# Optimization experiments

Hardware: AMD Instinct MI355X
Metric: run time of the kernel (lower is better)

## Reference

```python
import jax, jax.numpy as jnp
import numpy as np

N, D_IN, D_BLOCK, D_OUT, E, K = 65536, 128, 256, 128, 8, 2


def setup_inputs() -> dict:
    key = jax.random.key(0)
    ks = jax.random.split(key, 8)
    s_in = 1.0 / np.sqrt(D_IN)
    s_h = 1.0 / np.sqrt(D_BLOCK)
    return {
        "x": jax.random.normal(ks[0], (N, D_IN), jnp.float32),
        "Wg": jax.random.normal(ks[1], (D_IN, E), jnp.float32) * s_in,
        "W1": jax.random.normal(ks[2], (E, D_IN, D_BLOCK), jnp.float32) * s_in,
        "b1": jax.random.normal(ks[3], (E, D_BLOCK), jnp.float32) * 0.01,
        "W2": jax.random.normal(ks[4], (E, D_BLOCK, D_BLOCK), jnp.float32) * s_h,
        "b2": jax.random.normal(ks[5], (E, D_BLOCK), jnp.float32) * 0.01,
        "Wo": jax.random.normal(ks[6], (D_BLOCK, D_OUT), jnp.float32) * s_h,
        "bo": jax.random.normal(ks[7], (D_OUT,), jnp.float32) * 0.01,
    }


def reference(x, Wg, W1, b1, W2, b2, Wo, bo):
    # Router: linear gate -> top-k -> softmax over the k selected logits,
    # scattered back to a dense [N, E] combine-weight matrix (zeros elsewhere).
    logits = x @ Wg                                   # [N, E]
    topv, topi = jax.lax.top_k(logits, K)             # [N, K]
    w_topk = jax.nn.softmax(topv, axis=-1)            # [N, K]
    onehot = jax.nn.one_hot(topi, E, dtype=x.dtype)   # [N, K, E]
    weights = jnp.einsum("nk,nke->ne", w_topk, onehot)  # [N, E]

    # Expert MLPs (n_blocks=2, ReLU, dropout=0 at eval), computed for all
    # experts over all tokens; unselected experts have weight 0, so the
    # weighted combine reproduces the original masked gather/scatter math.
    h = jax.nn.relu(jnp.einsum("nd,edh->enh", x, W1) + b1[:, None, :])   # [E,N,H]
    h = jax.nn.relu(jnp.einsum("enh,ehg->eng", h, W2) + b2[:, None, :])  # [E,N,H]
    y = jnp.einsum("enh,ho->eno", h, Wo) + bo                             # [E,N,O]

    # Weighted scatter-add combine: outs[n] = sum_e weights[n,e] * y[e,n]
    return jnp.einsum("ne,eno->no", weights, y)
```

## Files before the change

### kernel.cpp

```cpp
#include <hip/hip_runtime.h>
#include <math.h>

typedef unsigned short ushort_t;
typedef __attribute__((ext_vector_type(8))) short bf16x8;
typedef __attribute__((ext_vector_type(4))) float f32x4;
typedef __attribute__((ext_vector_type(8))) unsigned short u16x8;

#define N_TOK 65536
#define DIN 128
#define HD 256
#define DOUT 128
#define NEXP 8
#define MT 64
#define NSEG 32
#define SEGCAP 2048
#define SEGTILES (SEGCAP / MT)

__device__ __forceinline__ unsigned short f2bf(float f) {
    union { float f; unsigned int i; } v; v.f = f;
    unsigned int i = v.i;
    return (unsigned short)((i + 0x7FFFu + ((i >> 16) & 1u)) >> 16);
}

__global__ void pack_weights(const float* __restrict__ W1,
                             const float* __restrict__ W2,
                             const float* __restrict__ Wo,
                             ushort_t* __restrict__ wt1f,
                             ushort_t* __restrict__ wt2f,
                             ushort_t* __restrict__ wotf,
                             int* __restrict__ segcnt) {
    if (blockIdx.x == 0) segcnt[threadIdx.x] = 0;
    int id = blockIdx.x * 256 + threadIdx.x;
    const float* src; ushort_t* dst; int Nn, ksteps, c;
    if (id < 32768) {
        int e = id >> 12; c = id & 4095;
        Nn = HD; ksteps = 4; src = W1 + (size_t)e * DIN * HD; dst = wt1f + (size_t)id * 8;
    } else if (id < 98304) {
        int t = id - 32768; int e = t >> 13; c = t & 8191;
        Nn = HD; ksteps = 8; src = W2 + (size_t)e * HD * HD; dst = wt2f + (size_t)t * 8;
    } else {
        int t = id - 98304; c = t;
        Nn = DOUT; ksteps = 8; src = Wo; dst = wotf + (size_t)t * 8;
    }
    int L = c & 63; int kc = c >> 6;
    int kstep = kc % ksteps; int ntile = kc / ksteps;
    int q = L >> 4, m = L & 15;
    int n = ntile * 16 + m; int k0 = kstep * 32 + q * 8;
    u16x8 v;
#pragma unroll
    for (int j = 0; j < 8; j++) v[j] = f2bf(src[(size_t)(k0 + j) * Nn + n]);
    *(u16x8*)dst = v;
}

#define RT_TPB 32
__global__ __launch_bounds__(256)
void router_kernel(const float* __restrict__ x,
                   const float* __restrict__ Wg,
                   int* __restrict__ segcnt,
                   int* __restrict__ list_tok,
                   float* __restrict__ list_w) {
    __shared__ float wgsT[NEXP * 132];
    __shared__ int lcnt[NEXP];
    __shared__ int lbase[NEXP];
    int tid = threadIdx.x;
    if (tid < NEXP) lcnt[tid] = 0;
    for (int i = tid; i < DIN * NEXP; i += 256) {
        int e = i & 7, k = i >> 3;
        wgsT[e * 132 + k] = Wg[i];
    }
    __syncthreads();

    int s = tid & 7;
    int tl = tid >> 3;
    int n = blockIdx.x * RT_TPB + tl;

    const float4* xr = (const float4*)(x + (size_t)n * DIN + s * 16);
    float4 xv[4];
#pragma unroll
    for (int j = 0; j < 4; j++) xv[j] = xr[j];

    float lg[NEXP];
#pragma unroll
    for (int e = 0; e < NEXP; e++) {
        const float4* wp = (const float4*)(wgsT + e * 132 + s * 16);
        float a = 0.f;
#pragma unroll
        for (int j = 0; j < 4; j++) {
            float4 wv = wp[j];
            a += xv[j].x * wv.x + xv[j].y * wv.y + xv[j].z * wv.z + xv[j].w * wv.w;
        }
        lg[e] = a;
    }
#pragma unroll
    for (int d = 1; d < 8; d <<= 1) {
#pragma unroll
        for (int e = 0; e < NEXP; e++) lg[e] += __shfl_xor(lg[e], d, 64);
    }
    int e0 = 0; float v0 = lg[0];
#pragma unroll
    for (int e = 1; e < NEXP; e++) if (lg[e] > v0) { v0 = lg[e]; e0 = e; }
    int e1 = -1; float v1 = -3.0e38f;
#pragma unroll
    for (int e = 0; e < NEXP; e++) if (e != e0 && lg[e] > v1) { v1 = lg[e]; e1 = e; }
    float t = expf(v1 - v0);
    float inv = 1.0f / (1.0f + t);
    float w0 = inv, w1 = t * inv;

    bool writer = (s == 0);
    int p0 = 0, p1 = 0;
    if (writer) {
        p0 = atomicAdd(&lcnt[e0], 1);
        p1 = atomicAdd(&lcnt[e1], 1);
    }
    __syncthreads();
    int c = blockIdx.x & (NSEG - 1);
    if (tid < NEXP) lbase[tid] = atomicAdd(&segcnt[tid * NSEG + c], lcnt[tid]);
    __syncthreads();
    if (writer) {
        int q0 = lbase[e0] + p0;
        int idx0 = (e0 * NSEG + c) * SEGCAP + q0;
        list_tok[idx0] = n;
        list_w[idx0] = w0;
        int q1 = lbase[e1] + p1;
        int idx1 = (e1 * NSEG + c) * SEGCAP + q1;
        list_tok[idx1] = n;
        list_w[idx1] = w1;
    }
}

__global__ void init_out(const float* __restrict__ bo, float* __restrict__ out) {
    int gid = blockIdx.x * 256 + threadIdx.x;
    float4 b = ((const float4*)bo)[gid & 31];
    ((float4*)out)[gid] = b;
}

__global__ __launch_bounds__(256, 3)
void expert_kernel(const float* __restrict__ x,
                   const int* __restrict__ segcnt,
                   const int* __restrict__ list_tok,
                   const float* __restrict__ list_w,
                   const ushort_t* __restrict__ wt1f,
                   const ushort_t* __restrict__ wt2f,
                   const ushort_t* __restrict__ wotf,
                   const float* __restrict__ b1,
                   const float* __restrict__ b2,
                   float* __restrict__ out) {
    int bid = blockIdx.x;
    int e = bid & 7;
    int c = (bid >> 3) & (NSEG - 1);
    int t = bid >> 8;
    int cnt = segcnt[e * NSEG + c];
    int base = t * MT;
    if (base >= cnt) return;
    int rows = cnt - base; if (rows > MT) rows = MT;
    int lidx = (e * NSEG + c) * SEGCAP + base;

    __shared__ __align__(16) ushort_t bufA[8192];
    __shared__ __align__(16) ushort_t bufH[16384];
    __shared__ int toks_s[MT];
    __shared__ float wts_s[MT];

    int tid = threadIdx.x;
    int lane = tid & 63;
    int w = tid >> 6;
    int q = lane >> 4;
    int mcol = lane & 15;

    if (tid < MT) {
        int rr = tid < rows ? tid : rows - 1;
        toks_s[tid] = list_tok[lidx + rr];
        wts_s[tid] = list_w[lidx + rr];
    }
    for (int cc = tid; cc < 1024; cc += 256) {
        int row = cc >> 4;
        int kchunk = cc & 15;
        int rr = row < rows ? row : rows - 1;
        int tok = list_tok[lidx + rr];
        const float4* src = (const float4*)(x + (size_t)tok * DIN + kchunk * 8);
        float4 lo = src[0], hi = src[1];
        u16x8 v;
        v[0] = f2bf(lo.x); v[1] = f2bf(lo.y); v[2] = f2bf(lo.z); v[3] = f2bf(lo.w);
        v[4] = f2bf(hi.x); v[5] = f2bf(hi.y); v[6] = f2bf(hi.z); v[7] = f2bf(hi.w);
        int kstep = kchunk >> 2, qq = kchunk & 3;
        int dchunk = (kstep * 4 + (row >> 4)) * 64 + qq * 16 + (row & 15);
        ((u16x8*)bufA)[dchunk] = v;
    }
    __syncthreads();

    const bf16x8* Albs = (const bf16x8*)bufA;
    const bf16x8* Hlbs = (const bf16x8*)bufH;

    f32x4 acc[4][4];
#pragma unroll
    for (int mt = 0; mt < 4; mt++)
#pragma unroll
        for (int nt = 0; nt < 4; nt++) acc[mt][nt] = (f32x4){0.f, 0.f, 0.f, 0.f};
    const bf16x8* B1 = (const bf16x8*)(wt1f + (size_t)e * 4096 * 8);
#pragma unroll
    for (int kstep = 0; kstep < 4; kstep++) {
        bf16x8 a[4];
#pragma unroll
        for (int mt = 0; mt < 4; mt++) a[mt] = Albs[(kstep * 4 + mt) * 64 + lane];
#pragma unroll
        for (int nt = 0; nt < 4; nt++) {
            bf16x8 b = B1[((w * 4 + nt) * 4 + kstep) * 64 + lane];
#pragma unroll
            for (int mt = 0; mt < 4; mt++)
                acc[mt][nt] = __builtin_amdgcn_mfma_f32_16x16x32_bf16(a[mt], b, acc[mt][nt], 0, 0, 0);
        }
    }
#pragma unroll
    for (int nt = 0; nt < 4; nt++) {
        int nn = (w * 4 + nt) * 16 + mcol;
        float bias = b1[e * HD + nn];
        int kstep = nn >> 5, qq = (nn >> 3) & 3, jj = nn & 7;
#pragma unroll
        for (int mt = 0; mt < 4; mt++) {
#pragma unroll
            for (int r = 0; r < 4; r++) {
                float v = acc[mt][nt][r] + bias;
                v = v > 0.f ? v : 0.f;
                int chunk = (kstep * 4 + mt) * 64 + qq * 16 + q * 4 + r;
                bufH[chunk * 8 + jj] = f2bf(v);
            }
        }
    }
    __syncthreads();

    f32x4 acc2[4][4];
#pragma unroll
    for (int mt = 0; mt < 4; mt++)
#pragma unroll
        for (int nt = 0; nt < 4; nt++) acc2[mt][nt] = (f32x4){0.f, 0.f, 0.f, 0.f};
    const bf16x8* B2 = (const bf16x8*)(wt2f + (size_t)e * 8192 * 8);
#pragma unroll
    for (int kstep = 0; kstep < 8; kstep++) {
        bf16x8 a[4];
#pragma unroll
        for (int mt = 0; mt < 4; mt++) a[mt] = Hlbs[(kstep * 4 + mt) * 64 + lane];
#pragma unroll
        for (int nt = 0; nt < 4; nt++) {
            bf16x8 b = B2[((w * 4 + nt) * 8 + kstep) * 64 + lane];
#pragma unroll
            for (int mt = 0; mt < 4; mt++)
                acc2[mt][nt] = __builtin_amdgcn_mfma_f32_16x16x32_bf16(a[mt], b, acc2[mt][nt], 0, 0, 0);
        }
    }
    __syncthreads();
#pragma unroll
    for (int nt = 0; nt < 4; nt++) {
        int nn = (w * 4 + nt) * 16 + mcol;
        float bias = b2[e * HD + nn];
        int kstep = nn >> 5, qq = (nn >> 3) & 3, jj = nn & 7;
#pragma unroll
        for (int mt = 0; mt < 4; mt++) {
#pragma unroll
            for (int r = 0; r < 4; r++) {
                float v = acc2[mt][nt][r] + bias;
                v = v > 0.f ? v : 0.f;
                int chunk = (kstep * 4 + mt) * 64 + qq * 16 + q * 4 + r;
                bufH[chunk * 8 + jj] = f2bf(v);
            }
        }
    }
    __syncthreads();

    f32x4 acc3[4][2];
#pragma unroll
    for (int mt = 0; mt < 4; mt++)
#pragma unroll
        for (int nt = 0; nt < 2; nt++) acc3[mt][nt] = (f32x4){0.f, 0.f, 0.f, 0.f};
    const bf16x8* B3 = (const bf16x8*)wotf;
#pragma unroll
    for (int kstep = 0; kstep < 8; kstep++) {
        bf16x8 a[4];
#pragma unroll
        for (int mt = 0; mt < 4; mt++) a[mt] = Hlbs[(kstep * 4 + mt) * 64 + lane];
#pragma unroll
        for (int nt = 0; nt < 2; nt++) {
            bf16x8 b = B3[((w * 2 + nt) * 8 + kstep) * 64 + lane];
#pragma unroll
            for (int mt = 0; mt < 4; mt++)
                acc3[mt][nt] = __builtin_amdgcn_mfma_f32_16x16x32_bf16(a[mt], b, acc3[mt][nt], 0, 0, 0);
        }
    }
#pragma unroll
    for (int mt = 0; mt < 4; mt++) {
#pragma unroll
        for (int r = 0; r < 4; r++) {
            int row = mt * 16 + q * 4 + r;
            if (row < rows) {
                int tok = toks_s[row];
                float wgt = wts_s[row];
                float* dst = out + (size_t)tok * DOUT;
#pragma unroll
                for (int nt = 0; nt < 2; nt++) {
                    int col = (w * 2 + nt) * 16 + mcol;
                    atomicAdd(&dst[col], wgt * acc3[mt][nt][r]);
                }
            }
        }
    }
}

extern "C" void kernel_launch(void* const* d_in, const int* in_sizes, int n_in,
                              void* d_out, int out_size, void* d_ws, size_t ws_size,
                              hipStream_t stream) {
    const float* x  = (const float*)d_in[0];
    const float* Wg = (const float*)d_in[1];
    const float* W1 = (const float*)d_in[2];
    const float* b1 = (const float*)d_in[3];
    const float* W2 = (const float*)d_in[4];
    const float* b2 = (const float*)d_in[5];
    const float* Wo = (const float*)d_in[6];
    const float* bo = (const float*)d_in[7];
    float* out = (float*)d_out;

    char* ws = (char*)d_ws;
    size_t off = 0;
    int* segcnt    = (int*)(ws + off);    off += 1024;
    int* list_tok  = (int*)(ws + off);    off += (size_t)NEXP * NSEG * SEGCAP * 4;
    float* list_w  = (float*)(ws + off);  off += (size_t)NEXP * NSEG * SEGCAP * 4;
    ushort_t* wt1f = (ushort_t*)(ws + off); off += (size_t)NEXP * DIN * HD * 2;
    ushort_t* wt2f = (ushort_t*)(ws + off); off += (size_t)NEXP * HD * HD * 2;
    ushort_t* wotf = (ushort_t*)(ws + off); off += (size_t)HD * DOUT * 2;

    pack_weights<<<400, 256, 0, stream>>>(W1, W2, Wo, wt1f, wt2f, wotf, segcnt);
    router_kernel<<<N_TOK / RT_TPB, 256, 0, stream>>>(x, Wg, segcnt, list_tok, list_w);
    init_out<<<(N_TOK * DOUT / 4) / 256, 256, 0, stream>>>(bo, out);
    expert_kernel<<<NEXP * NSEG * SEGTILES, 256, 0, stream>>>(x, segcnt, list_tok, list_w,
                                                              wt1f, wt2f, wotf, b1, b2, out);
}
```

Measured before the change: 213.8 us.

## Fuse prep kernels into one launch and halve expert tile rows for occupancy

Merges weight packing, routing, and output bias initialization into a single prep kernel that dispatches on block index, and zeroes the segment counters with a memset instead. The expert kernel's token tile shrinks from 64 to 32 rows, which halves shared memory and accumulator registers so launch bounds can request 6 blocks per SM instead of 3. The smaller tiles double the grid and halve the reuse of each weight fragment loaded from global memory, so weight traffic per token increases.

```diff
diff --git a/kernel.cpp b/kernel.cpp
--- a/kernel.cpp
+++ b/kernel.cpp
@@ -11,10 +11,14 @@
 #define HD 256
 #define DOUT 128
 #define NEXP 8
-#define MT 64
+#define MT 32
 #define NSEG 32
 #define SEGCAP 2048
 #define SEGTILES (SEGCAP / MT)
+
+#define G_INIT 8192
+#define G_ROUTER 2048
+#define G_PACK 400
 
 __device__ __forceinline__ unsigned short f2bf(float f) {
     union { float f; unsigned int i; } v; v.f = f;
@@ -22,25 +26,111 @@
     return (unsigned short)((i + 0x7FFFu + ((i >> 16) & 1u)) >> 16);
 }
 
-__global__ void pack_weights(const float* __restrict__ W1,
-                             const float* __restrict__ W2,
-                             const float* __restrict__ Wo,
-                             ushort_t* __restrict__ wt1f,
-                             ushort_t* __restrict__ wt2f,
-                             ushort_t* __restrict__ wotf,
-                             int* __restrict__ segcnt) {
-    if (blockIdx.x == 0) segcnt[threadIdx.x] = 0;
-    int id = blockIdx.x * 256 + threadIdx.x;
+#define RT_TPB 32
+__global__ __launch_bounds__(256)
+void prep_kernel(const float* __restrict__ x,
+                 const float* __restrict__ Wg,
+                 const float* __restrict__ W1,
+                 const float* __restrict__ W2,
+                 const float* __restrict__ Wo,
+                 const float* __restrict__ bo,
+                 int* __restrict__ segcnt,
+                 int* __restrict__ list_tok,
+                 float* __restrict__ list_w,
+                 ushort_t* __restrict__ wt1f,
+                 ushort_t* __restrict__ wt2f,
+                 ushort_t* __restrict__ wotf,
+                 float* __restrict__ out) {
+    int tid = threadIdx.x;
+    int bx = blockIdx.x;
+
+    if (bx < G_INIT) {
+        int gid = bx * 256 + tid;
+        float4 b = ((const float4*)bo)[gid & 31];
+        ((float4*)out)[gid] = b;
+        return;
+    }
+    if (bx < G_INIT + G_ROUTER) {
+        int rb = bx - G_INIT;
+        __shared__ float wgsT[NEXP * 132];
+        __shared__ int lcnt[NEXP];
+        __shared__ int lbase[NEXP];
+        if (tid < NEXP) lcnt[tid] = 0;
+        for (int i = tid; i < DIN * NEXP; i += 256) {
+            int e = i & 7, k = i >> 3;
+            wgsT[e * 132 + k] = Wg[i];
+        }
+        __syncthreads();
+
+        int s = tid & 7;
+        int tl = tid >> 3;
+        int n = rb * RT_TPB + tl;
+
+        const float4* xr = (const float4*)(x + (size_t)n * DIN + s * 16);
+        float4 xv[4];
+#pragma unroll
+        for (int j = 0; j < 4; j++) xv[j] = xr[j];
+
+        float lg[NEXP];
+#pragma unroll
+        for (int e = 0; e < NEXP; e++) {
+            const float4* wp = (const float4*)(wgsT + e * 132 + s * 16);
+            float a = 0.f;
+#pragma unroll
+            for (int j = 0; j < 4; j++) {
+                float4 wv = wp[j];
+                a += xv[j].x * wv.x + xv[j].y * wv.y + xv[j].z * wv.z + xv[j].w * wv.w;
+            }
+            lg[e] = a;
+        }
+#pragma unroll
+        for (int d = 1; d < 8; d <<= 1) {
+#pragma unroll
+            for (int e = 0; e < NEXP; e++) lg[e] += __shfl_xor(lg[e], d, 64);
+        }
+        int e0 = 0; float v0 = lg[0];
+#pragma unroll
+        for (int e = 1; e < NEXP; e++) if (lg[e] > v0) { v0 = lg[e]; e0 = e; }
+        int e1 = -1; float v1 = -3.0e38f;
+#pragma unroll
+        for (int e = 0; e < NEXP; e++) if (e != e0 && lg[e] > v1) { v1 = lg[e]; e1 = e; }
+        float t = expf(v1 - v0);
+        float inv = 1.0f / (1.0f + t);
+        float w0 = inv, w1 = t * inv;
+
+        bool writer = (s == 0);
+        int p0 = 0, p1 = 0;
+        if (writer) {
+            p0 = atomicAdd(&lcnt[e0], 1);
+            p1 = atomicAdd(&lcnt[e1], 1);
+        }
+        __syncthreads();
+        int c = rb & (NSEG - 1);
+        if (tid < NEXP) lbase[tid] = atomicAdd(&segcnt[tid * NSEG + c], lcnt[tid]);
+        __syncthreads();
+        if (writer) {
+            int q0 = lbase[e0] + p0;
+            int idx0 = (e0 * NSEG + c) * SEGCAP + q0;
+            list_tok[idx0] = n;
+            list_w[idx0] = w0;
+            int q1 = lbase[e1] + p1;
+            int idx1 = (e1 * NSEG + c) * SEGCAP + q1;
+            list_tok[idx1] = n;
+            list_w[idx1] = w1;
+        }
+        return;
+    }
+    int id = (bx - G_INIT - G_ROUTER) * 256 + tid;
     const float* src; ushort_t* dst; int Nn, ksteps, c;
     if (id < 32768) {
         int e = id >> 12; c = id & 4095;
         Nn = HD; ksteps = 4; src = W1 + (size_t)e * DIN * HD; dst = wt1f + (size_t)id * 8;
     } else if (id < 98304) {
-        int t = id - 32768; int e = t >> 13; c = t & 8191;
-        Nn = HD; ksteps = 8; src = W2 + (size_t)e * HD * HD; dst = wt2f + (size_t)t * 8;
+        int t2 = id - 32768; int e = t2 >> 13; c = t2 & 8191;
+        Nn = HD; ksteps = 8; src = W2 + (size_t)e * HD * HD; dst = wt2f + (size_t)t2 * 8;
     } else {
-        int t = id - 98304; c = t;
-        Nn = DOUT; ksteps = 8; src = Wo; dst = wotf + (size_t)t * 8;
+        int t2 = id - 98304; c = t2;
+        Nn = DOUT; ksteps = 8; src = Wo; dst = wotf + (size_t)t2 * 8;
     }
     int L = c & 63; int kc = c >> 6;
     int kstep = kc % ksteps; int ntile = kc / ksteps;
@@ -52,89 +142,7 @@
     *(u16x8*)dst = v;
 }
 
-#define RT_TPB 32
-__global__ __launch_bounds__(256)
-void router_kernel(const float* __restrict__ x,
-                   const float* __restrict__ Wg,
-                   int* __restrict__ segcnt,
-                   int* __restrict__ list_tok,
-                   float* __restrict__ list_w) {
-    __shared__ float wgsT[NEXP * 132];
-    __shared__ int lcnt[NEXP];
-    __shared__ int lbase[NEXP];
-    int tid = threadIdx.x;
-    if (tid < NEXP) lcnt[tid] = 0;
-    for (int i = tid; i < DIN * NEXP; i += 256) {
-        int e = i & 7, k = i >> 3;
-        wgsT[e * 132 + k] = Wg[i];
-    }
-    __syncthreads();
-
-    int s = tid & 7;
-    int tl = tid >> 3;
-    int n = blockIdx.x * RT_TPB + tl;
-
-    const float4* xr = (const float4*)(x + (size_t)n * DIN + s * 16);
-    float4 xv[4];
-#pragma unroll
-    for (int j = 0; j < 4; j++) xv[j] = xr[j];
-
-    float lg[NEXP];
-#pragma unroll
-    for (int e = 0; e < NEXP; e++) {
-        const float4* wp = (const float4*)(wgsT + e * 132 + s * 16);
-        float a = 0.f;
-#pragma unroll
-        for (int j = 0; j < 4; j++) {
-            float4 wv = wp[j];
-            a += xv[j].x * wv.x + xv[j].y * wv.y + xv[j].z * wv.z + xv[j].w * wv.w;
-        }
-        lg[e] = a;
-    }
-#pragma unroll
-    for (int d = 1; d < 8; d <<= 1) {
-#pragma unroll
-        for (int e = 0; e < NEXP; e++) lg[e] += __shfl_xor(lg[e], d, 64);
-    }
-    int e0 = 0; float v0 = lg[0];
-#pragma unroll
-    for (int e = 1; e < NEXP; e++) if (lg[e] > v0) { v0 = lg[e]; e0 = e; }
-    int e1 = -1; float v1 = -3.0e38f;
-#pragma unroll
-    for (int e = 0; e < NEXP; e++) if (e != e0 && lg[e] > v1) { v1 = lg[e]; e1 = e; }
-    float t = expf(v1 - v0);
-    float inv = 1.0f / (1.0f + t);
-    float w0 = inv, w1 = t * inv;
-
-    bool writer = (s == 0);
-    int p0 = 0, p1 = 0;
-    if (writer) {
-        p0 = atomicAdd(&lcnt[e0], 1);
-        p1 = atomicAdd(&lcnt[e1], 1);
-    }
-    __syncthreads();
-    int c = blockIdx.x & (NSEG - 1);
-    if (tid < NEXP) lbase[tid] = atomicAdd(&segcnt[tid * NSEG + c], lcnt[tid]);
-    __syncthreads();
-    if (writer) {
-        int q0 = lbase[e0] + p0;
-        int idx0 = (e0 * NSEG + c) * SEGCAP + q0;
-        list_tok[idx0] = n;
-        list_w[idx0] = w0;
-        int q1 = lbase[e1] + p1;
-        int idx1 = (e1 * NSEG + c) * SEGCAP + q1;
-        list_tok[idx1] = n;
-        list_w[idx1] = w1;
-    }
-}
-
-__global__ void init_out(const float* __restrict__ bo, float* __restrict__ out) {
-    int gid = blockIdx.x * 256 + threadIdx.x;
-    float4 b = ((const float4*)bo)[gid & 31];
-    ((float4*)out)[gid] = b;
-}
-
-__global__ __launch_bounds__(256, 3)
+__global__ __launch_bounds__(256, 6)
 void expert_kernel(const float* __restrict__ x,
                    const int* __restrict__ segcnt,
                    const int* __restrict__ list_tok,
@@ -155,8 +163,8 @@
     int rows = cnt - base; if (rows > MT) rows = MT;
     int lidx = (e * NSEG + c) * SEGCAP + base;
 
-    __shared__ __align__(16) ushort_t bufA[8192];
-    __shared__ __align__(16) ushort_t bufH[16384];
+    __shared__ __align__(16) ushort_t bufA[4096];
+    __shared__ __align__(16) ushort_t bufH[8192];
     __shared__ int toks_s[MT];
     __shared__ float wts_s[MT];
 
@@ -171,7 +179,7 @@
         toks_s[tid] = list_tok[lidx + rr];
         wts_s[tid] = list_w[lidx + rr];
     }
-    for (int cc = tid; cc < 1024; cc += 256) {
+    for (int cc = tid; cc < 512; cc += 256) {
         int row = cc >> 4;
         int kchunk = cc & 15;
         int rr = row < rows ? row : rows - 1;
@@ -182,7 +190,7 @@
         v[0] = f2bf(lo.x); v[1] = f2bf(lo.y); v[2] = f2bf(lo.z); v[3] = f2bf(lo.w);
         v[4] = f2bf(hi.x); v[5] = f2bf(hi.y); v[6] = f2bf(hi.z); v[7] = f2bf(hi.w);
         int kstep = kchunk >> 2, qq = kchunk & 3;
-        int dchunk = (kstep * 4 + (row >> 4)) * 64 + qq * 16 + (row & 15);
+        int dchunk = (kstep * 2 + (row >> 4)) * 64 + qq * 16 + (row & 15);
         ((u16x8*)bufA)[dchunk] = v;
     }
     __syncthreads();
@@ -190,22 +198,22 @@
     const bf16x8* Albs = (const bf16x8*)bufA;
     const bf16x8* Hlbs = (const bf16x8*)bufH;
 
-    f32x4 acc[4][4];
-#pragma unroll
-    for (int mt = 0; mt < 4; mt++)
+    f32x4 acc[2][4];
+#pragma unroll
+    for (int mt = 0; mt < 2; mt++)
 #pragma unroll
         for (int nt = 0; nt < 4; nt++) acc[mt][nt] = (f32x4){0.f, 0.f, 0.f, 0.f};
     const bf16x8* B1 = (const bf16x8*)(wt1f + (size_t)e * 4096 * 8);
 #pragma unroll
     for (int kstep = 0; kstep < 4; kstep++) {
-        bf16x8 a[4];
-#pragma unroll
-        for (int mt = 0; mt < 4; mt++) a[mt] = Albs[(kstep * 4 + mt) * 64 + lane];
+        bf16x8 a[2];
+#pragma unroll
+        for (int mt = 0; mt < 2; mt++) a[mt] = Albs[(kstep * 2 + mt) * 64 + lane];
 #pragma unroll
         for (int nt = 0; nt < 4; nt++) {
             bf16x8 b = B1[((w * 4 + nt) * 4 + kstep) * 64 + lane];
 #pragma unroll
-            for (int mt = 0; mt < 4; mt++)
+            for (int mt = 0; mt < 2; mt++)
                 acc[mt][nt] = __builtin_amdgcn_mfma_f32_16x16x32_bf16(a[mt], b, acc[mt][nt], 0, 0, 0);
         }
     }
@@ -215,34 +223,34 @@
         float bias = b1[e * HD + nn];
         int kstep = nn >> 5, qq = (nn >> 3) & 3, jj = nn & 7;
 #pragma unroll
-        for (int mt = 0; mt < 4; mt++) {
+        for (int mt = 0; mt < 2; mt++) {
 #pragma unroll
             for (int r = 0; r < 4; r++) {
                 float v = acc[mt][nt][r] + bias;
                 v = v > 0.f ? v : 0.f;
-                int chunk = (kstep * 4 + mt) * 64 + qq * 16 + q * 4 + r;
+                int chunk = (kstep * 2 + mt) * 64 + qq * 16 + q * 4 + r;
                 bufH[chunk * 8 + jj] = f2bf(v);
             }
         }
     }
     __syncthreads();
 
-    f32x4 acc2[4][4];
-#pragma unroll
-    for (int mt = 0; mt < 4; mt++)
+    f32x4 acc2[2][4];
+#pragma unroll
+    for (int mt = 0; mt < 2; mt++)
 #pragma unroll
         for (int nt = 0; nt < 4; nt++) acc2[mt][nt] = (f32x4){0.f, 0.f, 0.f, 0.f};
     const bf16x8* B2 = (const bf16x8*)(wt2f + (size_t)e * 8192 * 8);
 #pragma unroll
     for (int kstep = 0; kstep < 8; kstep++) {
-        bf16x8 a[4];
-#pragma unroll
-        for (int mt = 0; mt < 4; mt++) a[mt] = Hlbs[(kstep * 4 + mt) * 64 + lane];
+        bf16x8 a[2];
+#pragma unroll
+        for (int mt = 0; mt < 2; mt++) a[mt] = Hlbs[(kstep * 2 + mt) * 64 + lane];
 #pragma unroll
         for (int nt = 0; nt < 4; nt++) {
             bf16x8 b = B2[((w * 4 + nt) * 8 + kstep) * 64 + lane];
 #pragma unroll
-            for (int mt = 0; mt < 4; mt++)
+            for (int mt = 0; mt < 2; mt++)
                 acc2[mt][nt] = __builtin_amdgcn_mfma_f32_16x16x32_bf16(a[mt], b, acc2[mt][nt], 0, 0, 0);
         }
     }
@@ -253,39 +261,39 @@
         float bias = b2[e * HD + nn];
         int kstep = nn >> 5, qq = (nn >> 3) & 3, jj = nn & 7;
 #pragma unroll
-        for (int mt = 0; mt < 4; mt++) {
+        for (int mt = 0; mt < 2; mt++) {
 #pragma unroll
             for (int r = 0; r < 4; r++) {
                 float v = acc2[mt][nt][r] + bias;
                 v = v > 0.f ? v : 0.f;
-                int chunk = (kstep * 4 + mt) * 64 + qq * 16 + q * 4 + r;
+                int chunk = (kstep * 2 + mt) * 64 + qq * 16 + q * 4 + r;
                 bufH[chunk * 8 + jj] = f2bf(v);
             }
         }
     }
     __syncthreads();
 
-    f32x4 acc3[4][2];
-#pragma unroll
-    for (int mt = 0; mt < 4; mt++)
+    f32x4 acc3[2][2];
+#pragma unroll
+    for (int mt = 0; mt < 2; mt++)
 #pragma unroll
         for (int nt = 0; nt < 2; nt++) acc3[mt][nt] = (f32x4){0.f, 0.f, 0.f, 0.f};
     const bf16x8* B3 = (const bf16x8*)wotf;
 #pragma unroll
     for (int kstep = 0; kstep < 8; kstep++) {
-        bf16x8 a[4];
-#pragma unroll
-        for (int mt = 0; mt < 4; mt++) a[mt] = Hlbs[(kstep * 4 + mt) * 64 + lane];
+        bf16x8 a[2];
+#pragma unroll
+        for (int mt = 0; mt < 2; mt++) a[mt] = Hlbs[(kstep * 2 + mt) * 64 + lane];
 #pragma unroll
         for (int nt = 0; nt < 2; nt++) {
             bf16x8 b = B3[((w * 2 + nt) * 8 + kstep) * 64 + lane];
 #pragma unroll
-            for (int mt = 0; mt < 4; mt++)
+            for (int mt = 0; mt < 2; mt++)
                 acc3[mt][nt] = __builtin_amdgcn_mfma_f32_16x16x32_bf16(a[mt], b, acc3[mt][nt], 0, 0, 0);
         }
     }
 #pragma unroll
-    for (int mt = 0; mt < 4; mt++) {
+    for (int mt = 0; mt < 2; mt++) {
 #pragma unroll
         for (int r = 0; r < 4; r++) {
             int row = mt * 16 + q * 4 + r;
@@ -325,9 +333,9 @@
     ushort_t* wt2f = (ushort_t*)(ws + off); off += (size_t)NEXP * HD * HD * 2;
     ushort_t* wotf = (ushort_t*)(ws + off); off += (size_t)HD * DOUT * 2;
 
-    pack_weights<<<400, 256, 0, stream>>>(W1, W2, Wo, wt1f, wt2f, wotf, segcnt);
-    router_kernel<<<N_TOK / RT_TPB, 256, 0, stream>>>(x, Wg, segcnt, list_tok, list_w);
-    init_out<<<(N_TOK * DOUT / 4) / 256, 256, 0, stream>>>(bo, out);
-    expert_kernel<<<NEXP * NSEG * SEGTILES, 256, 0, stream>>>(x, segcnt, list_tok, list_w,
-                                                              wt1f, wt2f, wotf, b1, b2, out);
+    hipMemsetAsync(segcnt, 0, 1024, stream);
+    prep_kernel<<<G_INIT + G_ROUTER + G_PACK, 256, 0, stream>>>(
+        x, Wg, W1, W2, Wo, bo, segcnt, list_tok, list_w, wt1f, wt2f, wotf, out);
+    expert_kernel<<<NEXP * NSEG * SEGTILES, 256, 0, stream>>>(
+        x, segcnt, list_tok, list_w, wt1f, wt2f, wotf, b1, b2, out);
 }
```

New measurement: 213.3 us. Within noise of the previous version (-0.3%).

## Fuse init, router and weight-pack kernels; prefetch MFMA B fragments in registers

Applied to the files above, without the earlier changes.

Merges the output-bias init, router and weight-packing kernels into one prep kernel that dispatches on block index, and replaces the in-kernel segcnt zeroing with a memset. This cuts launches and lets the three independent stages run concurrently. The expert kernel also double-buffers B-operand loads for the first two GEMMs and preloads all Wo fragments before the third GEMM, so global loads overlap with MFMA work. The extra live registers (up to 16 bf16x8 for Wo) may raise pressure under the 3-wave occupancy bound.

```diff
diff --git a/kernel.cpp b/kernel.cpp
--- a/kernel.cpp
+++ b/kernel.cpp
@@ -16,31 +16,121 @@
 #define SEGCAP 2048
 #define SEGTILES (SEGCAP / MT)
 
+#define G_INIT 8192
+#define G_ROUTER 2048
+#define G_PACK 400
+
 __device__ __forceinline__ unsigned short f2bf(float f) {
     union { float f; unsigned int i; } v; v.f = f;
     unsigned int i = v.i;
     return (unsigned short)((i + 0x7FFFu + ((i >> 16) & 1u)) >> 16);
 }
 
-__global__ void pack_weights(const float* __restrict__ W1,
-                             const float* __restrict__ W2,
-                             const float* __restrict__ Wo,
-                             ushort_t* __restrict__ wt1f,
-                             ushort_t* __restrict__ wt2f,
-                             ushort_t* __restrict__ wotf,
-                             int* __restrict__ segcnt) {
-    if (blockIdx.x == 0) segcnt[threadIdx.x] = 0;
-    int id = blockIdx.x * 256 + threadIdx.x;
+#define RT_TPB 32
+__global__ __launch_bounds__(256)
+void prep_kernel(const float* __restrict__ x,
+                 const float* __restrict__ Wg,
+                 const float* __restrict__ W1,
+                 const float* __restrict__ W2,
+                 const float* __restrict__ Wo,
+                 const float* __restrict__ bo,
+                 int* __restrict__ segcnt,
+                 int* __restrict__ list_tok,
+                 float* __restrict__ list_w,
+                 ushort_t* __restrict__ wt1f,
+                 ushort_t* __restrict__ wt2f,
+                 ushort_t* __restrict__ wotf,
+                 float* __restrict__ out) {
+    int tid = threadIdx.x;
+    int bx = blockIdx.x;
+
+    if (bx < G_INIT) {
+        int gid = bx * 256 + tid;
+        float4 b = ((const float4*)bo)[gid & 31];
+        ((float4*)out)[gid] = b;
+        return;
+    }
+    if (bx < G_INIT + G_ROUTER) {
+        int rb = bx - G_INIT;
+        __shared__ float wgsT[NEXP * 132];
+        __shared__ int lcnt[NEXP];
+        __shared__ int lbase[NEXP];
+        if (tid < NEXP) lcnt[tid] = 0;
+        for (int i = tid; i < DIN * NEXP; i += 256) {
+            int e = i & 7, k = i >> 3;
+            wgsT[e * 132 + k] = Wg[i];
+        }
+        __syncthreads();
+
+        int s = tid & 7;
+        int tl = tid >> 3;
+        int n = rb * RT_TPB + tl;
+
+        const float4* xr = (const float4*)(x + (size_t)n * DIN + s * 16);
+        float4 xv[4];
+#pragma unroll
+        for (int j = 0; j < 4; j++) xv[j] = xr[j];
+
+        float lg[NEXP];
+#pragma unroll
+        for (int e = 0; e < NEXP; e++) {
+            const float4* wp = (const float4*)(wgsT + e * 132 + s * 16);
+            float a = 0.f;
+#pragma unroll
+            for (int j = 0; j < 4; j++) {
+                float4 wv = wp[j];
+                a += xv[j].x * wv.x + xv[j].y * wv.y + xv[j].z * wv.z + xv[j].w * wv.w;
+            }
+            lg[e] = a;
+        }
+#pragma unroll
+        for (int d = 1; d < 8; d <<= 1) {
+#pragma unroll
+            for (int e = 0; e < NEXP; e++) lg[e] += __shfl_xor(lg[e], d, 64);
+        }
+        int e0 = 0; float v0 = lg[0];
+#pragma unroll
+        for (int e = 1; e < NEXP; e++) if (lg[e] > v0) { v0 = lg[e]; e0 = e; }
+        int e1 = -1; float v1 = -3.0e38f;
+#pragma unroll
+        for (int e = 0; e < NEXP; e++) if (e != e0 && lg[e] > v1) { v1 = lg[e]; e1 = e; }
+        float t = expf(v1 - v0);
+        float inv = 1.0f / (1.0f + t);
+        float w0 = inv, w1 = t * inv;
+
+        bool writer = (s == 0);
+        int p0 = 0, p1 = 0;
+        if (writer) {
+            p0 = atomicAdd(&lcnt[e0], 1);
+            p1 = atomicAdd(&lcnt[e1], 1);
+        }
+        __syncthreads();
+        int c = rb & (NSEG - 1);
+        if (tid < NEXP) lbase[tid] = atomicAdd(&segcnt[tid * NSEG + c], lcnt[tid]);
+        __syncthreads();
+        if (writer) {
+            int q0 = lbase[e0] + p0;
+            int idx0 = (e0 * NSEG + c) * SEGCAP + q0;
+            list_tok[idx0] = n;
+            list_w[idx0] = w0;
+            int q1 = lbase[e1] + p1;
+            int idx1 = (e1 * NSEG + c) * SEGCAP + q1;
+            list_tok[idx1] = n;
+            list_w[idx1] = w1;
+        }
+        return;
+    }
+    int id = (bx - G_INIT - G_ROUTER) * 256 + tid;
     const float* src; ushort_t* dst; int Nn, ksteps, c;
     if (id < 32768) {
         int e = id >> 12; c = id & 4095;
         Nn = HD; ksteps = 4; src = W1 + (size_t)e * DIN * HD; dst = wt1f + (size_t)id * 8;
     } else if (id < 98304) {
-        int t = id - 32768; int e = t >> 13; c = t & 8191;
-        Nn = HD; ksteps = 8; src = W2 + (size_t)e * HD * HD; dst = wt2f + (size_t)t * 8;
+        int t2 = id - 32768; int e = t2 >> 13; c = t2 & 8191;
+        Nn = HD; ksteps = 8; src = W2 + (size_t)e * HD * HD; dst = wt2f + (size_t)t2 * 8;
     } else {
-        int t = id - 98304; c = t;
-        Nn = DOUT; ksteps = 8; src = Wo; dst = wotf + (size_t)t * 8;
+        int t2 = id - 98304; c = t2;
+        Nn = DOUT; ksteps = 8; src = Wo; dst = wotf + (size_t)t2 * 8;
     }
     int L = c & 63; int kc = c >> 6;
     int kstep = kc % ksteps; int ntile = kc / ksteps;
@@ -50,88 +140,6 @@
 #pragma unroll
     for (int j = 0; j < 8; j++) v[j] = f2bf(src[(size_t)(k0 + j) * Nn + n]);
     *(u16x8*)dst = v;
-}
-
-#define RT_TPB 32
-__global__ __launch_bounds__(256)
-void router_kernel(const float* __restrict__ x,
-                   const float* __restrict__ Wg,
-                   int* __restrict__ segcnt,
-                   int* __restrict__ list_tok,
-                   float* __restrict__ list_w) {
-    __shared__ float wgsT[NEXP * 132];
-    __shared__ int lcnt[NEXP];
-    __shared__ int lbase[NEXP];
-    int tid = threadIdx.x;
-    if (tid < NEXP) lcnt[tid] = 0;
-    for (int i = tid; i < DIN * NEXP; i += 256) {
-        int e = i & 7, k = i >> 3;
-        wgsT[e * 132 + k] = Wg[i];
-    }
-    __syncthreads();
-
-    int s = tid & 7;
-    int tl = tid >> 3;
-    int n = blockIdx.x * RT_TPB + tl;
-
-    const float4* xr = (const float4*)(x + (size_t)n * DIN + s * 16);
-    float4 xv[4];
-#pragma unroll
-    for (int j = 0; j < 4; j++) xv[j] = xr[j];
-
-    float lg[NEXP];
-#pragma unroll
-    for (int e = 0; e < NEXP; e++) {
-        const float4* wp = (const float4*)(wgsT + e * 132 + s * 16);
-        float a = 0.f;
-#pragma unroll
-        for (int j = 0; j < 4; j++) {
-            float4 wv = wp[j];
-            a += xv[j].x * wv.x + xv[j].y * wv.y + xv[j].z * wv.z + xv[j].w * wv.w;
-        }
-        lg[e] = a;
-    }
-#pragma unroll
-    for (int d = 1; d < 8; d <<= 1) {
-#pragma unroll
-        for (int e = 0; e < NEXP; e++) lg[e] += __shfl_xor(lg[e], d, 64);
-    }
-    int e0 = 0; float v0 = lg[0];
-#pragma unroll
-    for (int e = 1; e < NEXP; e++) if (lg[e] > v0) { v0 = lg[e]; e0 = e; }
-    int e1 = -1; float v1 = -3.0e38f;
-#pragma unroll
-    for (int e = 0; e < NEXP; e++) if (e != e0 && lg[e] > v1) { v1 = lg[e]; e1 = e; }
-    float t = expf(v1 - v0);
-    float inv = 1.0f / (1.0f + t);
-    float w0 = inv, w1 = t * inv;
-
-    bool writer = (s == 0);
-    int p0 = 0, p1 = 0;
-    if (writer) {
-        p0 = atomicAdd(&lcnt[e0], 1);
-        p1 = atomicAdd(&lcnt[e1], 1);
-    }
-    __syncthreads();
-    int c = blockIdx.x & (NSEG - 1);
-    if (tid < NEXP) lbase[tid] = atomicAdd(&segcnt[tid * NSEG + c], lcnt[tid]);
-    __syncthreads();
-    if (writer) {
-        int q0 = lbase[e0] + p0;
-        int idx0 = (e0 * NSEG + c) * SEGCAP + q0;
-        list_tok[idx0] = n;
-        list_w[idx0] = w0;
-        int q1 = lbase[e1] + p1;
-        int idx1 = (e1 * NSEG + c) * SEGCAP + q1;
-        list_tok[idx1] = n;
-        list_w[idx1] = w1;
-    }
-}
-
-__global__ void init_out(const float* __restrict__ bo, float* __restrict__ out) {
-    int gid = blockIdx.x * 256 + threadIdx.x;
-    float4 b = ((const float4*)bo)[gid & 31];
-    ((float4*)out)[gid] = b;
 }
 
 __global__ __launch_bounds__(256, 3)
@@ -166,6 +174,14 @@
     int q = lane >> 4;
     int mcol = lane & 15;
 
+    const bf16x8* B1 = (const bf16x8*)(wt1f + (size_t)e * 4096 * 8);
+    const bf16x8* B2 = (const bf16x8*)(wt2f + (size_t)e * 8192 * 8);
+    const bf16x8* B3 = (const bf16x8*)wotf;
+
+    bf16x8 b1c[4], b1n[4];
+#pragma unroll
+    for (int nt = 0; nt < 4; nt++) b1c[nt] = B1[((w * 4 + nt) * 4 + 0) * 64 + lane];
+
     if (tid < MT) {
         int rr = tid < rows ? tid : rows - 1;
         toks_s[tid] = list_tok[lidx + rr];
@@ -195,19 +211,23 @@
     for (int mt = 0; mt < 4; mt++)
 #pragma unroll
         for (int nt = 0; nt < 4; nt++) acc[mt][nt] = (f32x4){0.f, 0.f, 0.f, 0.f};
-    const bf16x8* B1 = (const bf16x8*)(wt1f + (size_t)e * 4096 * 8);
 #pragma unroll
     for (int kstep = 0; kstep < 4; kstep++) {
+        if (kstep < 3) {
+#pragma unroll
+            for (int nt = 0; nt < 4; nt++)
+                b1n[nt] = B1[((w * 4 + nt) * 4 + kstep + 1) * 64 + lane];
+        }
         bf16x8 a[4];
 #pragma unroll
         for (int mt = 0; mt < 4; mt++) a[mt] = Albs[(kstep * 4 + mt) * 64 + lane];
 #pragma unroll
-        for (int nt = 0; nt < 4; nt++) {
-            bf16x8 b = B1[((w * 4 + nt) * 4 + kstep) * 64 + lane];
+        for (int nt = 0; nt < 4; nt++)
 #pragma unroll
             for (int mt = 0; mt < 4; mt++)
-                acc[mt][nt] = __builtin_amdgcn_mfma_f32_16x16x32_bf16(a[mt], b, acc[mt][nt], 0, 0, 0);
-        }
+                acc[mt][nt] = __builtin_amdgcn_mfma_f32_16x16x32_bf16(a[mt], b1c[nt], acc[mt][nt], 0, 0, 0);
+#pragma unroll
+        for (int nt = 0; nt < 4; nt++) b1c[nt] = b1n[nt];
     }
 #pragma unroll
     for (int nt = 0; nt < 4; nt++) {
@@ -225,6 +245,9 @@
             }
         }
     }
+    bf16x8 b2c[4], b2n[4];
+#pragma unroll
+    for (int nt = 0; nt < 4; nt++) b2c[nt] = B2[((w * 4 + nt) * 8 + 0) * 64 + lane];
     __syncthreads();
 
     f32x4 acc2[4][4];
@@ -232,20 +255,30 @@
     for (int mt = 0; mt < 4; mt++)
 #pragma unroll
         for (int nt = 0; nt < 4; nt++) acc2[mt][nt] = (f32x4){0.f, 0.f, 0.f, 0.f};
-    const bf16x8* B2 = (const bf16x8*)(wt2f + (size_t)e * 8192 * 8);
 #pragma unroll
     for (int kstep = 0; kstep < 8; kstep++) {
+        if (kstep < 7) {
+#pragma unroll
+            for (int nt = 0; nt < 4; nt++)
+                b2n[nt] = B2[((w * 4 + nt) * 8 + kstep + 1) * 64 + lane];
+        }
         bf16x8 a[4];
 #pragma unroll
         for (int mt = 0; mt < 4; mt++) a[mt] = Hlbs[(kstep * 4 + mt) * 64 + lane];
 #pragma unroll
-        for (int nt = 0; nt < 4; nt++) {
-            bf16x8 b = B2[((w * 4 + nt) * 8 + kstep) * 64 + lane];
+        for (int nt = 0; nt < 4; nt++)
 #pragma unroll
             for (int mt = 0; mt < 4; mt++)
-                acc2[mt][nt] = __builtin_amdgcn_mfma_f32_16x16x32_bf16(a[mt], b, acc2[mt][nt], 0, 0, 0);
-        }
-    }
+                acc2[mt][nt] = __builtin_amdgcn_mfma_f32_16x16x32_bf16(a[mt], b2c[nt], acc2[mt][nt], 0, 0, 0);
+#pragma unroll
+        for (int nt = 0; nt < 4; nt++) b2c[nt] = b2n[nt];
+    }
+    bf16x8 b3f[16];
+#pragma unroll
+    for (int kstep = 0; kstep < 8; kstep++)
+#pragma unroll
+        for (int nt = 0; nt < 2; nt++)
+            b3f[kstep * 2 + nt] = B3[((w * 2 + nt) * 8 + kstep) * 64 + lane];
     __syncthreads();
 #pragma unroll
     for (int nt = 0; nt < 4; nt++) {
@@ -270,19 +303,16 @@
     for (int mt = 0; mt < 4; mt++)
 #pragma unroll
         for (int nt = 0; nt < 2; nt++) acc3[mt][nt] = (f32x4){0.f, 0.f, 0.f, 0.f};
-    const bf16x8* B3 = (const bf16x8*)wotf;
 #pragma unroll
     for (int kstep = 0; kstep < 8; kstep++) {
         bf16x8 a[4];
 #pragma unroll
         for (int mt = 0; mt < 4; mt++) a[mt] = Hlbs[(kstep * 4 + mt) * 64 + lane];
 #pragma unroll
-        for (int nt = 0; nt < 2; nt++) {
-            bf16x8 b = B3[((w * 2 + nt) * 8 + kstep) * 64 + lane];
+        for (int nt = 0; nt < 2; nt++)
 #pragma unroll
             for (int mt = 0; mt < 4; mt++)
-                acc3[mt][nt] = __builtin_amdgcn_mfma_f32_16x16x32_bf16(a[mt], b, acc3[mt][nt], 0, 0, 0);
-        }
+                acc3[mt][nt] = __builtin_amdgcn_mfma_f32_16x16x32_bf16(a[mt], b3f[kstep * 2 + nt], acc3[mt][nt], 0, 0, 0);
     }
 #pragma unroll
     for (int mt = 0; mt < 4; mt++) {
@@ -325,9 +355,9 @@
     ushort_t* wt2f = (ushort_t*)(ws + off); off += (size_t)NEXP * HD * HD * 2;
     ushort_t* wotf = (ushort_t*)(ws + off); off += (size_t)HD * DOUT * 2;
 
-    pack_weights<<<400, 256, 0, stream>>>(W1, W2, Wo, wt1f, wt2f, wotf, segcnt);
-    router_kernel<<<N_TOK / RT_TPB, 256, 0, stream>>>(x, Wg, segcnt, list_tok, list_w);
-    init_out<<<(N_TOK * DOUT / 4) / 256, 256, 0, stream>>>(bo, out);
-    expert_kernel<<<NEXP * NSEG * SEGTILES, 256, 0, stream>>>(x, segcnt, list_tok, list_w,
-                                                              wt1f, wt2f, wotf, b1, b2, out);
+    hipMemsetAsync(segcnt, 0, 1024, stream);
+    prep_kernel<<<G_INIT + G_ROUTER + G_PACK, 256, 0, stream>>>(
+        x, Wg, W1, W2, Wo, bo, segcnt, list_tok, list_w, wt1f, wt2f, wotf, out);
+    expert_kernel<<<NEXP * NSEG * SEGTILES, 256, 0, stream>>>(
+        x, segcnt, list_tok, list_w, wt1f, wt2f, wotf, b1, b2, out);
 }
```

New measurement: 208.1 us. 1.03x faster.
